# Performance work log

Measured on AMD Instinct MI355X. Metric: run time of the kernel, lower is better.

## Reference

```python
import jax, jax.numpy as jnp
import numpy as np

NUM_NODES = 25
EMBED_DIM = 64
OUT_SIZE = 2
N_TOTAL = 204800   # 8192 graphs * 25 nodes
N_EDGES = 3276800  # avg degree 16


def setup_inputs() -> dict:
    key = jax.random.key(0)
    ks = jax.random.split(key, 8)
    x = jax.random.normal(ks[0], (N_TOTAL, EMBED_DIM), dtype=jnp.float32)
    # random edges; real graphs are graph-local but math is identical
    edge_index = jax.random.randint(ks[1], (2, N_EDGES), 0, N_TOTAL, dtype=jnp.int32)
    batch = jnp.repeat(jnp.arange(N_TOTAL // NUM_NODES, dtype=jnp.int32), NUM_NODES)
    hid = NUM_NODES * EMBED_DIM  # 1600
    W_conv = jax.random.normal(ks[2], (EMBED_DIM, EMBED_DIM), dtype=jnp.float32) / np.sqrt(EMBED_DIM)
    b_conv = jnp.zeros((EMBED_DIM,), dtype=jnp.float32)
    W1 = jax.random.normal(ks[3], (hid, hid), dtype=jnp.float32) / np.sqrt(hid)
    b1 = jnp.zeros((hid,), dtype=jnp.float32)
    W2 = jax.random.normal(ks[4], (hid, OUT_SIZE), dtype=jnp.float32) / np.sqrt(hid)
    b2 = jnp.zeros((OUT_SIZE,), dtype=jnp.float32)
    return {"x": x, "edge_index": edge_index, "batch": batch,
            "W_conv": W_conv, "b_conv": b_conv,
            "W1": W1, "b1": b1, "W2": W2, "b2": b2}


def reference(x, edge_index, batch, W_conv, b_conv, W1, b1, W2, b2):
    N = x.shape[0]
    # --- GCNConv: add self-loops, symmetric degree norm, transform, scatter-add ---
    loop = jnp.arange(N, dtype=edge_index.dtype)
    src = jnp.concatenate([edge_index[0], loop])
    dst = jnp.concatenate([edge_index[1], loop])
    deg = jax.ops.segment_sum(jnp.ones_like(dst, dtype=x.dtype), dst, num_segments=N)
    dinv = jax.lax.rsqrt(deg)  # deg >= 1 due to self-loops
    norm = dinv[src] * dinv[dst]                       # [E+N]
    h = x @ W_conv                                     # [N, D]
    msg = h[src] * norm[:, None]                       # gather + scale
    h = jax.ops.segment_sum(msg, dst, num_segments=N) + b_conv
    h = jax.nn.relu(h)
    # --- dense head ---
    nb = -(-batch.shape[0] // NUM_NODES)               # ceil
    h = h.reshape(nb, NUM_NODES * EMBED_DIM)           # [B, 1600]
    h = jax.nn.relu(h @ W1 + b1)
    logits = h @ W2 + b2
    return jax.nn.softmax(logits, axis=-1)
```

## Files before the change

kernel.cpp:

```cpp
#include <hip/hip_runtime.h>
#include <hip/hip_bf16.h>
#include <stdint.h>

#define NT   204800
#define NE   3276800
#define ED   64
#define NBG  8192
#define HID  1600
#define HPAD 1664
#define CAP  56
#define NBKT 400
#define BCAP 9216

typedef float  f32x4  __attribute__((ext_vector_type(4)));
typedef __bf16 bf16x8 __attribute__((ext_vector_type(8)));

__device__ __forceinline__ void async_ld16(const void* g, void* l) {
    __builtin_amdgcn_global_load_lds(
        (__attribute__((address_space(1))) const void*)g,
        (__attribute__((address_space(3))) void*)l, 16, 0, 0);
}

__device__ __forceinline__ unsigned short f2bf_raw(float f) {
    __hip_bfloat16 h = __float2bfloat16(f);
    return *(unsigned short*)&h;
}

__global__ void k_initg(int* __restrict__ gcur) {
    int t = threadIdx.x;
    if (t < NBKT) gcur[t] = t * BCAP;
}

__global__ __launch_bounds__(256) void k_part(const int* __restrict__ srcv,
                                              const int* __restrict__ dstv,
                                              int* __restrict__ gcur,
                                              unsigned* __restrict__ rec) {
    __shared__ int hist[NBKT];
    __shared__ int gofs[NBKT];
    const int t = threadIdx.x;
    const int base = blockIdx.x * (NE / 512);
    for (int i = t; i < NBKT; i += 256) hist[i] = 0;
    __syncthreads();
    unsigned keep[25];
#pragma unroll
    for (int j = 0; j < 25; ++j) {
        int d = dstv[base + j * 256 + t];
        int b = d >> 9;
        int ls = atomicAdd(&hist[b], 1);
        keep[j] = ((unsigned)ls << 18) | ((unsigned)(d & 511) << 9) | (unsigned)b;
    }
    __syncthreads();
    for (int i = t; i < NBKT; i += 256) gofs[i] = atomicAdd(&gcur[i], hist[i]);
    __syncthreads();
#pragma unroll
    for (int j = 0; j < 25; ++j) {
        int s = srcv[base + j * 256 + t];
        unsigned k = keep[j];
        int b   = (int)(k & 511u);
        int rel = (int)((k >> 9) & 511u);
        int idx = gofs[b] + (int)(k >> 18);
        if (idx < (b + 1) * BCAP)
            rec[idx] = ((unsigned)s << 9) | (unsigned)rel;
    }
}

__global__ __launch_bounds__(512) void k_fillb(const int* __restrict__ gcur,
                                               const unsigned* __restrict__ rec,
                                               int* __restrict__ cur,
                                               int* __restrict__ csr,
                                               float* __restrict__ dinv) {
    __shared__ int cnt[512];
    const int t = threadIdx.x;
    const int b = blockIdx.x;
    const int n0 = b * 512;
    cnt[t] = 0;
    __syncthreads();
    const int bstart = b * BCAP;
    int bcnt = gcur[b] - bstart;
    bcnt = (bcnt > BCAP) ? BCAP : bcnt;
    for (int idx = t; idx < bcnt; idx += 512) {
        unsigned r = rec[bstart + idx];
        unsigned rel = r & 511u;
        int ls = atomicAdd(&cnt[rel], 1);
        if (ls < CAP) csr[(size_t)(n0 + rel) * CAP + ls] = (int)(r >> 9);
    }
    __syncthreads();
    int cn = cnt[t];
    cur[n0 + t] = cn;
    dinv[n0 + t] = rsqrtf((float)cn + 1.f);
}

__global__ __launch_bounds__(256) void k_gemm_conv(const float* __restrict__ x,
                                                   const float* __restrict__ Wc,
                                                   const float* __restrict__ dinv,
                                                   __hip_bfloat16* __restrict__ hbs) {
    __shared__ unsigned short Xs[64 * 72];
    __shared__ unsigned short Wt[64 * 72];
    const int t = threadIdx.x;
    const int row0 = blockIdx.x * 64;
#pragma unroll
    for (int i = 0; i < 4; ++i) {
        int idx = i * 256 + t;
        int r = idx >> 4, c4 = (idx & 15) << 2;
        f32x4 wv = ((const f32x4*)Wc)[idx];
        Wt[(c4 + 0) * 72 + r] = f2bf_raw(wv.x);
        Wt[(c4 + 1) * 72 + r] = f2bf_raw(wv.y);
        Wt[(c4 + 2) * 72 + r] = f2bf_raw(wv.z);
        Wt[(c4 + 3) * 72 + r] = f2bf_raw(wv.w);
        f32x4 xv = ((const f32x4*)(x + (size_t)row0 * 64))[idx];
        ushort4 p;
        p.x = f2bf_raw(xv.x);
        p.y = f2bf_raw(xv.y);
        p.z = f2bf_raw(xv.z);
        p.w = f2bf_raw(xv.w);
        *(ushort4*)&Xs[r * 72 + c4] = p;
    }
    __syncthreads();
    const int w = t >> 6, lane = t & 63;
    const int fr = lane & 15, fq = lane >> 4;
    f32x4 acc[4] = {};
#pragma unroll
    for (int kb = 0; kb < 2; ++kb) {
        bf16x8 av = *(const bf16x8*)&Xs[(w * 16 + fr) * 72 + kb * 32 + fq * 8];
#pragma unroll
        for (int j = 0; j < 4; ++j) {
            bf16x8 bv = *(const bf16x8*)&Wt[(j * 16 + fr) * 72 + kb * 32 + fq * 8];
            acc[j] = __builtin_amdgcn_mfma_f32_16x16x32_bf16(av, bv, acc[j], 0, 0, 0);
        }
    }
#pragma unroll
    for (int r = 0; r < 4; ++r) {
        int row = row0 + w * 16 + fq * 4 + r;
        float di = dinv[row];
        unsigned short* dst = (unsigned short*)&hbs[(size_t)row * 64];
#pragma unroll
        for (int j = 0; j < 4; ++j)
            dst[j * 16 + fr] = f2bf_raw(acc[j][r] * di);
    }
}

__global__ __launch_bounds__(1024) void k_gather(const int* __restrict__ cur,
                                                 const int* __restrict__ csr,
                                                 const float* __restrict__ dinv,
                                                 const __hip_bfloat16* __restrict__ hbs,
                                                 const float* __restrict__ bc,
                                                 __hip_bfloat16* __restrict__ Hb) {
    const int lane = threadIdx.x & 63;
    const int du = __builtin_amdgcn_readfirstlane(blockIdx.x * 16 + (threadIdx.x >> 6));
    const float di = dinv[du];
    int cn = cur[du];
    cn = (cn > CAP) ? CAP : cn;
    const int* __restrict__ lst = csr + (size_t)du * CAP;
    float acc = __bfloat162float(hbs[(size_t)du * ED + lane]);
    int e = 0;
    for (; e + 16 <= cn; e += 16) {
#pragma unroll
        for (int q = 0; q < 16; ++q) {
            int s = lst[e + q];
            acc += __bfloat162float(hbs[(size_t)s * ED + lane]);
        }
    }
    if (cn & 8) {
#pragma unroll
        for (int q = 0; q < 8; ++q) {
            int s = lst[e + q];
            acc += __bfloat162float(hbs[(size_t)s * ED + lane]);
        }
        e += 8;
    }
    if (cn & 4) {
#pragma unroll
        for (int q = 0; q < 4; ++q) {
            int s = lst[e + q];
            acc += __bfloat162float(hbs[(size_t)s * ED + lane]);
        }
        e += 4;
    }
    if (cn & 2) {
#pragma unroll
        for (int q = 0; q < 2; ++q) {
            int s = lst[e + q];
            acc += __bfloat162float(hbs[(size_t)s * ED + lane]);
        }
        e += 2;
    }
    if (cn & 1) {
        int s = lst[e];
        acc += __bfloat162float(hbs[(size_t)s * ED + lane]);
    }
    Hb[(size_t)du * ED + lane] = __float2bfloat16(fmaxf(bc[lane] + di * acc, 0.f));
}

__global__ void k_convW1(const float* __restrict__ W1, __hip_bfloat16* __restrict__ Bt) {
    __shared__ float tile[64][65];
    const int t = threadIdx.x;
    const int k0 = blockIdx.x * 64;
    const int n0 = blockIdx.y * 64;
#pragma unroll
    for (int i = 0; i < 16; ++i) {
        int lin = i * 256 + t;
        int r = lin >> 6, c = lin & 63;
        int n = n0 + c;
        tile[r][c] = (n < HID) ? W1[(size_t)(k0 + r) * HID + n] : 0.f;
    }
    __syncthreads();
#pragma unroll
    for (int i = 0; i < 16; ++i) {
        int lin = i * 256 + t;
        int nn = lin >> 6, kk = lin & 63;
        Bt[(size_t)(n0 + nn) * HID + k0 + kk] = __float2bfloat16(tile[kk][nn]);
    }
}

__global__ __launch_bounds__(256) void k_gemm1(const __hip_bfloat16* __restrict__ A,
                                               const __hip_bfloat16* __restrict__ Bt,
                                               const float* __restrict__ b1,
                                               __hip_bfloat16* __restrict__ h2) {
    __shared__ unsigned short As[128 * 32];
    __shared__ unsigned short Bs[128 * 32];
    const int t = threadIdx.x;
    const int lane = t & 63;
    const int wave = t >> 6;
    const int bm0 = blockIdx.x * 128;
    const int bn0 = blockIdx.y * 128;
    const int wm = (wave >> 1) * 64;
    const int wn = (wave & 1) * 64;
    const int fr = lane & 15;
    const int fq = lane >> 4;
    const int sr = t >> 2;
    const int scs = (((t & 3) ^ ((sr >> 1) & 3)) * 8);
    const __hip_bfloat16* ga0 = A + (size_t)(bm0 + sr) * HID + scs;
    const __hip_bfloat16* ga1 = A + (size_t)(bm0 + 64 + sr) * HID + scs;
    const __hip_bfloat16* gb0 = Bt + (size_t)(bn0 + sr) * HID + scs;
    const __hip_bfloat16* gb1 = Bt + (size_t)(bn0 + 64 + sr) * HID + scs;
    unsigned short* lA0 = &As[t * 8];
    unsigned short* lA1 = &As[(256 + t) * 8];
    unsigned short* lB0 = &Bs[t * 8];
    unsigned short* lB1 = &Bs[(256 + t) * 8];
    const int rdx = (fr >> 1) & 3;
    const unsigned short* fa0 = &As[(wm + fr) * 32 + (fq ^ rdx) * 8];
    const unsigned short* fb0 = &Bs[(wn + fr) * 32 + (fq ^ rdx) * 8];
    f32x4 acc[4][4] = {};
    for (int k0 = 0; k0 < HID; k0 += 32) {
        async_ld16(ga0, lA0); async_ld16(ga1, lA1);
        async_ld16(gb0, lB0); async_ld16(gb1, lB1);
        ga0 += 32; ga1 += 32; gb0 += 32; gb1 += 32;
        __syncthreads();
        bf16x8 av[4], bv[4];
#pragma unroll
        for (int i = 0; i < 4; ++i) av[i] = *(const bf16x8*)(fa0 + i * 16 * 32);
#pragma unroll
        for (int j = 0; j < 4; ++j) bv[j] = *(const bf16x8*)(fb0 + j * 16 * 32);
#pragma unroll
        for (int i = 0; i < 4; ++i)
#pragma unroll
            for (int j = 0; j < 4; ++j)
                acc[i][j] = __builtin_amdgcn_mfma_f32_16x16x32_bf16(av[i], bv[j], acc[i][j], 0, 0, 0);
        __syncthreads();
    }
#pragma unroll
    for (int j = 0; j < 4; ++j) {
        int n = bn0 + wn + j * 16 + fr;
        if (n < HID) {
            float bias = b1[n];
#pragma unroll
            for (int i = 0; i < 4; ++i) {
#pragma unroll
                for (int r = 0; r < 4; ++r) {
                    int m = bm0 + wm + i * 16 + fq * 4 + r;
                    float v = acc[i][j][r] + bias;
                    h2[(size_t)m * HID + n] = __float2bfloat16(fmaxf(v, 0.f));
                }
            }
        }
    }
}

__global__ void k_head(const __hip_bfloat16* __restrict__ h2, const float* __restrict__ W2,
                       const float* __restrict__ b2, float* __restrict__ out) {
    int g = blockIdx.x * 4 + (threadIdx.x >> 6);
    int lane = threadIdx.x & 63;
    const __hip_bfloat16* row = h2 + (size_t)g * HID;
    float a0 = 0.f, a1 = 0.f;
#pragma unroll
    for (int i = 0; i < 25; ++i) {
        int k = i * 64 + lane;
        float hv = __bfloat162float(row[k]);
        float2 w = ((const float2*)W2)[k];
        a0 += hv * w.x;
        a1 += hv * w.y;
    }
#pragma unroll
    for (int off = 32; off > 0; off >>= 1) {
        a0 += __shfl_down(a0, off, 64);
        a1 += __shfl_down(a1, off, 64);
    }
    if (lane == 0) {
        float l0 = a0 + b2[0], l1 = a1 + b2[1];
        float mx = fmaxf(l0, l1);
        float e0 = expf(l0 - mx), e1 = expf(l1 - mx);
        float s = e0 + e1;
        out[2 * g]     = e0 / s;
        out[2 * g + 1] = e1 / s;
    }
}

extern "C" void kernel_launch(void* const* d_in, const int* in_sizes, int n_in,
                              void* d_out, int out_size, void* d_ws, size_t ws_size,
                              hipStream_t stream) {
    const float* x  = (const float*)d_in[0];
    const int*   ei = (const int*)d_in[1];
    const float* Wc = (const float*)d_in[3];
    const float* bc = (const float*)d_in[4];
    const float* W1 = (const float*)d_in[5];
    const float* b1 = (const float*)d_in[6];
    const float* W2 = (const float*)d_in[7];
    const float* b2 = (const float*)d_in[8];
    float* out = (float*)d_out;

    const int* srcv = ei;
    const int* dstv = ei + NE;

    char* ws = (char*)d_ws;
    int*   cur  = (int*)ws;
    float* dinv = (float*)(ws + 819200);
    int*   gcur = (int*)(ws + 1638400);
    int*   csr  = (int*)(ws + 1642496);
    unsigned* rec = (unsigned*)(ws + 47517696);
    __hip_bfloat16* hbs = (__hip_bfloat16*)(ws + 47517696);
    __hip_bfloat16* h2  = (__hip_bfloat16*)(ws + 47517696);
    __hip_bfloat16* Hb  = (__hip_bfloat16*)(ws + 73732096);
    __hip_bfloat16* Bt  = (__hip_bfloat16*)(ws + 99946496);

    k_initg    <<<1, 512, 0, stream>>>(gcur);
    k_part     <<<512, 256, 0, stream>>>(srcv, dstv, gcur, rec);
    k_fillb    <<<NBKT, 512, 0, stream>>>(gcur, rec, cur, csr, dinv);
    k_gemm_conv<<<NT / 64, 256, 0, stream>>>(x, Wc, dinv, hbs);
    k_gather   <<<NT / 16, 1024, 0, stream>>>(cur, csr, dinv, hbs, bc, Hb);
    k_convW1   <<<dim3(HID / 64, HPAD / 64), 256, 0, stream>>>(W1, Bt);
    k_gemm1    <<<dim3(NBG / 128, HPAD / 128), 256, 0, stream>>>(Hb, Bt, b1, h2);
    k_head     <<<NBG / 4, 256, 0, stream>>>(h2, W2, b2, out);
}
```

Before: 394.3 us.

## Double-buffer GEMM1 LDS tiles, swizzle block order, and pad gather tail

The dense GEMM gains two LDS buffers so the async global-to-LDS load of the next K tile overlaps the MFMAs on the current one, dropping one barrier per iteration. Its block index is remapped into groups of eight M tiles so concurrently running blocks share A and B rows in L2. The gather kernel moves to 256-thread blocks and replaces its 8/4/2/1 remainder branches with one padded 16-wide batch that reads the self row and subtracts it afterwards. The padding spends extra loads per node, and the double buffer doubles LDS use, which may lower occupancy.

```diff
diff --git a/kernel.cpp b/kernel.cpp
--- a/kernel.cpp
+++ b/kernel.cpp
@@ -139,19 +139,20 @@
     }
 }
 
-__global__ __launch_bounds__(1024) void k_gather(const int* __restrict__ cur,
-                                                 const int* __restrict__ csr,
-                                                 const float* __restrict__ dinv,
-                                                 const __hip_bfloat16* __restrict__ hbs,
-                                                 const float* __restrict__ bc,
-                                                 __hip_bfloat16* __restrict__ Hb) {
+__global__ __launch_bounds__(256) void k_gather(const int* __restrict__ cur,
+                                                const int* __restrict__ csr,
+                                                const float* __restrict__ dinv,
+                                                const __hip_bfloat16* __restrict__ hbs,
+                                                const float* __restrict__ bc,
+                                                __hip_bfloat16* __restrict__ Hb) {
     const int lane = threadIdx.x & 63;
-    const int du = __builtin_amdgcn_readfirstlane(blockIdx.x * 16 + (threadIdx.x >> 6));
+    const int du = __builtin_amdgcn_readfirstlane(blockIdx.x * 4 + (threadIdx.x >> 6));
     const float di = dinv[du];
     int cn = cur[du];
     cn = (cn > CAP) ? CAP : cn;
     const int* __restrict__ lst = csr + (size_t)du * CAP;
-    float acc = __bfloat162float(hbs[(size_t)du * ED + lane]);
+    const float self = __bfloat162float(hbs[(size_t)du * ED + lane]);
+    float acc = self;
     int e = 0;
     for (; e + 16 <= cn; e += 16) {
 #pragma unroll
@@ -160,33 +161,14 @@
             acc += __bfloat162float(hbs[(size_t)s * ED + lane]);
         }
     }
-    if (cn & 8) {
-#pragma unroll
-        for (int q = 0; q < 8; ++q) {
-            int s = lst[e + q];
+    if (e < cn) {
+        const int pad = e + 16 - cn;
+#pragma unroll
+        for (int q = 0; q < 16; ++q) {
+            int s = (e + q < cn) ? lst[e + q] : du;
             acc += __bfloat162float(hbs[(size_t)s * ED + lane]);
         }
-        e += 8;
-    }
-    if (cn & 4) {
-#pragma unroll
-        for (int q = 0; q < 4; ++q) {
-            int s = lst[e + q];
-            acc += __bfloat162float(hbs[(size_t)s * ED + lane]);
-        }
-        e += 4;
-    }
-    if (cn & 2) {
-#pragma unroll
-        for (int q = 0; q < 2; ++q) {
-            int s = lst[e + q];
-            acc += __bfloat162float(hbs[(size_t)s * ED + lane]);
-        }
-        e += 2;
-    }
-    if (cn & 1) {
-        int s = lst[e];
-        acc += __bfloat162float(hbs[(size_t)s * ED + lane]);
+        acc = fmaf(-(float)pad, self, acc);
     }
     Hb[(size_t)du * ED + lane] = __float2bfloat16(fmaxf(bc[lane] + di * acc, 0.f));
 }
@@ -216,13 +198,16 @@
                                                const __hip_bfloat16* __restrict__ Bt,
                                                const float* __restrict__ b1,
                                                __hip_bfloat16* __restrict__ h2) {
-    __shared__ unsigned short As[128 * 32];
-    __shared__ unsigned short Bs[128 * 32];
+    __shared__ unsigned short As[2][128 * 32];
+    __shared__ unsigned short Bs[2][128 * 32];
     const int t = threadIdx.x;
     const int lane = t & 63;
     const int wave = t >> 6;
-    const int bm0 = blockIdx.x * 128;
-    const int bn0 = blockIdx.y * 128;
+    const int lin = blockIdx.y * (NBG / 128) + blockIdx.x;
+    const int xc  = lin & 7;
+    const int pos = lin >> 3;
+    const int bm0 = (xc * 8 + (pos & 7)) * 128;
+    const int bn0 = (pos >> 3) * 128;
     const int wm = (wave >> 1) * 64;
     const int wn = (wave & 1) * 64;
     const int fr = lane & 15;
@@ -233,30 +218,51 @@
     const __hip_bfloat16* ga1 = A + (size_t)(bm0 + 64 + sr) * HID + scs;
     const __hip_bfloat16* gb0 = Bt + (size_t)(bn0 + sr) * HID + scs;
     const __hip_bfloat16* gb1 = Bt + (size_t)(bn0 + 64 + sr) * HID + scs;
-    unsigned short* lA0 = &As[t * 8];
-    unsigned short* lA1 = &As[(256 + t) * 8];
-    unsigned short* lB0 = &Bs[t * 8];
-    unsigned short* lB1 = &Bs[(256 + t) * 8];
     const int rdx = (fr >> 1) & 3;
-    const unsigned short* fa0 = &As[(wm + fr) * 32 + (fq ^ rdx) * 8];
-    const unsigned short* fb0 = &Bs[(wn + fr) * 32 + (fq ^ rdx) * 8];
+    const int fao = (wm + fr) * 32 + (fq ^ rdx) * 8;
+    const int fbo = (wn + fr) * 32 + (fq ^ rdx) * 8;
     f32x4 acc[4][4] = {};
-    for (int k0 = 0; k0 < HID; k0 += 32) {
-        async_ld16(ga0, lA0); async_ld16(ga1, lA1);
-        async_ld16(gb0, lB0); async_ld16(gb1, lB1);
+    async_ld16(ga0, &As[0][t * 8]);  async_ld16(ga1, &As[0][(256 + t) * 8]);
+    async_ld16(gb0, &Bs[0][t * 8]);  async_ld16(gb1, &Bs[0][(256 + t) * 8]);
+    ga0 += 32; ga1 += 32; gb0 += 32; gb1 += 32;
+    __syncthreads();
+    const int NKT = HID / 32;
+#pragma unroll 2
+    for (int kt = 0; kt < NKT - 1; ++kt) {
+        const int pc = kt & 1;
+        unsigned short* dA = &As[pc ^ 1][0];
+        unsigned short* dB = &Bs[pc ^ 1][0];
+        async_ld16(ga0, dA + t * 8);  async_ld16(ga1, dA + (256 + t) * 8);
+        async_ld16(gb0, dB + t * 8);  async_ld16(gb1, dB + (256 + t) * 8);
         ga0 += 32; ga1 += 32; gb0 += 32; gb1 += 32;
-        __syncthreads();
+        const unsigned short* fa = &As[pc][fao];
+        const unsigned short* fb = &Bs[pc][fbo];
         bf16x8 av[4], bv[4];
 #pragma unroll
-        for (int i = 0; i < 4; ++i) av[i] = *(const bf16x8*)(fa0 + i * 16 * 32);
-#pragma unroll
-        for (int j = 0; j < 4; ++j) bv[j] = *(const bf16x8*)(fb0 + j * 16 * 32);
+        for (int i = 0; i < 4; ++i) av[i] = *(const bf16x8*)(fa + i * 16 * 32);
+#pragma unroll
+        for (int j = 0; j < 4; ++j) bv[j] = *(const bf16x8*)(fb + j * 16 * 32);
 #pragma unroll
         for (int i = 0; i < 4; ++i)
 #pragma unroll
             for (int j = 0; j < 4; ++j)
                 acc[i][j] = __builtin_amdgcn_mfma_f32_16x16x32_bf16(av[i], bv[j], acc[i][j], 0, 0, 0);
         __syncthreads();
+    }
+    {
+        const int pe = (NKT - 1) & 1;
+        const unsigned short* fa = &As[pe][fao];
+        const unsigned short* fb = &Bs[pe][fbo];
+        bf16x8 av[4], bv[4];
+#pragma unroll
+        for (int i = 0; i < 4; ++i) av[i] = *(const bf16x8*)(fa + i * 16 * 32);
+#pragma unroll
+        for (int j = 0; j < 4; ++j) bv[j] = *(const bf16x8*)(fb + j * 16 * 32);
+#pragma unroll
+        for (int i = 0; i < 4; ++i)
+#pragma unroll
+            for (int j = 0; j < 4; ++j)
+                acc[i][j] = __builtin_amdgcn_mfma_f32_16x16x32_bf16(av[i], bv[j], acc[i][j], 0, 0, 0);
     }
 #pragma unroll
     for (int j = 0; j < 4; ++j) {
@@ -336,7 +342,7 @@
     k_part     <<<512, 256, 0, stream>>>(srcv, dstv, gcur, rec);
     k_fillb    <<<NBKT, 512, 0, stream>>>(gcur, rec, cur, csr, dinv);
     k_gemm_conv<<<NT / 64, 256, 0, stream>>>(x, Wc, dinv, hbs);
-    k_gather   <<<NT / 16, 1024, 0, stream>>>(cur, csr, dinv, hbs, bc, Hb);
+    k_gather   <<<NT / 4, 256, 0, stream>>>(cur, csr, dinv, hbs, bc, Hb);
     k_convW1   <<<dim3(HID / 64, HPAD / 64), 256, 0, stream>>>(W1, Bt);
     k_gemm1    <<<dim3(NBG / 128, HPAD / 128), 256, 0, stream>>>(Hb, Bt, b1, h2);
     k_head     <<<NBG / 4, 256, 0, stream>>>(h2, W2, b2, out);
```

Measured after the change: 395.6 us. Within noise of the previous version (+0.3%).
